# Kernel tuning notes

Hardware: AMD Instinct MI355X
Metric: run time of the kernel (lower is better)

Reference implementation:

```python
import jax, jax.numpy as jnp
import numpy as np

B, C, H, W = 16, 512, 48, 48


def setup_inputs() -> dict:
    key = jax.random.key(0)
    k1, k2 = jax.random.split(key)
    rgb = jax.random.normal(k1, (B, C, H, W), dtype=jnp.float32)
    depth = jax.random.normal(k2, (B, C, H, W), dtype=jnp.float32)
    return {"rgb": rgb, "depth": depth}


def reference(rgb, depth):
    b, c, h, w = rgb.shape
    hw = h * w
    q = rgb.reshape(b, c, hw)              # [B, C, HW]
    k = depth.reshape(b, c, hw)            # [B, C, HW]
    # channel-affinity: energy[b, i, j] = <rgb_chan_i, depth_chan_j>
    energy = jnp.einsum('bcn,bdn->bcd', q, k)   # [B, C, C]
    cl_index = jnp.argmax(energy, axis=2)       # [B, C] best-matching depth channel per rgb channel
    # gather matched depth channels and fuse
    gathered = depth[jnp.arange(b)[:, None], cl_index]  # [B, C, H, W]
    return rgb + gathered
```

## Files before the change

kernel.cpp:

```cpp
#include <hip/hip_runtime.h>
#include <stdint.h>

#define BATCH 16
#define CH    512
#define HW    2304
#define BM    128
#define BN    128

typedef _Float16 half8  __attribute__((ext_vector_type(8)));
typedef float    f32x16 __attribute__((ext_vector_type(16)));

#define MFMA16 __builtin_amdgcn_mfma_f32_32x32x16_f16

#define DELTA 3.5f

#define N_ELEM       ((size_t)BATCH * CH * HW)
#define ENERGY_ELEMS ((size_t)BATCH * CH * CH)
#define WS_FAST16    (ENERGY_ELEMS * 4 + 2 * N_ELEM * 2)

__device__ __forceinline__ uint32_t f32_sortable(float f) {
    uint32_t u = __float_as_uint(f);
    return (u & 0x80000000u) ? ~u : (u | 0x80000000u);
}

__global__ __launch_bounds__(256)
void cvt_f16_kernel(const float* __restrict__ rgb, const float* __restrict__ depth,
                    _Float16* __restrict__ rgb16, _Float16* __restrict__ depth16)
{
    const size_t stride = (size_t)gridDim.x * 256;
    for (size_t i = (size_t)blockIdx.x * 256 + threadIdx.x; i < N_ELEM / 8; i += stride) {
        float4 a0 = ((const float4*)rgb)[2 * i], a1 = ((const float4*)rgb)[2 * i + 1];
        half8 h;
        h[0] = (_Float16)a0.x; h[1] = (_Float16)a0.y;
        h[2] = (_Float16)a0.z; h[3] = (_Float16)a0.w;
        h[4] = (_Float16)a1.x; h[5] = (_Float16)a1.y;
        h[6] = (_Float16)a1.z; h[7] = (_Float16)a1.w;
        ((half8*)rgb16)[i] = h;
        float4 b0 = ((const float4*)depth)[2 * i], b1 = ((const float4*)depth)[2 * i + 1];
        half8 g;
        g[0] = (_Float16)b0.x; g[1] = (_Float16)b0.y;
        g[2] = (_Float16)b0.z; g[3] = (_Float16)b0.w;
        g[4] = (_Float16)b1.x; g[5] = (_Float16)b1.y;
        g[6] = (_Float16)b1.z; g[7] = (_Float16)b1.w;
        ((half8*)depth16)[i] = g;
    }
}


#define BK16    64
#define NKT16   (HW / BK16)
#define A16_OFF 0
#define B16_OFF 16384
#define BUF16_SZ 32768

__device__ __forceinline__ void dma16(const _Float16* g, char* l) {
    __builtin_amdgcn_global_load_lds(
        (const __attribute__((address_space(1))) void*)g,
        (__attribute__((address_space(3))) void*)l, 16, 0, 0);
}

__device__ __forceinline__ half8 rd16(const char* base, int r, int s0) {
    return *(const half8*)(base + r * 128 + ((s0 ^ ((r >> 1) & 7)) << 4));
}

__device__ __forceinline__ void compute16(const char* buf, int rA0, int rB, int hf,
                                          f32x16& acc0, f32x16& acc1) {
    __builtin_amdgcn_s_setprio(1);
    #pragma unroll
    for (int kc = 0; kc < 4; ++kc) {
        const int s0 = 2 * kc + hf;
        half8 a0 = rd16(buf + A16_OFF, rA0,      s0);
        half8 a1 = rd16(buf + A16_OFF, rA0 + 32, s0);
        half8 bb = rd16(buf + B16_OFF, rB,       s0);
        acc0 = MFMA16(a0, bb, acc0, 0, 0, 0);
        acc1 = MFMA16(a1, bb, acc1, 0, 0, 0);
    }
    __builtin_amdgcn_s_setprio(0);
}

__global__ __launch_bounds__(512, 1)
void screen16_kernel(const _Float16* __restrict__ q16,
                     const _Float16* __restrict__ k16,
                     float* __restrict__ energy)
{
    const int bid = blockIdx.x;
    const int nid = (bid & 7) * 32 + (bid >> 3);
    const int d0  = (nid & 3) * BN;
    const int c0  = ((nid >> 2) & 3) * BM;
    const int b   = nid >> 4;

    const int tid  = threadIdx.x;
    const int lane = tid & 63;
    const int w    = tid >> 6;
    const int wm   = w >> 2;
    const int wn   = w & 3;

    __shared__ __align__(16) char sm[2 * BUF16_SZ];

    const _Float16* qb = q16 + (size_t)b * CH * HW;
    const _Float16* kb = k16 + (size_t)b * CH * HW;

    const int lr = lane >> 3, ls = lane & 7;
    const int off0 = lr * HW + ((ls ^ (     (lr >> 1))) << 3);
    const int off1 = lr * HW + ((ls ^ (4 + (lr >> 1))) << 3);
    const _Float16* gA0 = qb + (size_t)(c0 + 16 * w)     * HW + off0;
    const _Float16* gA1 = qb + (size_t)(c0 + 16 * w + 8) * HW + off1;
    const _Float16* gB0 = kb + (size_t)(d0 + 16 * w)     * HW + off0;
    const _Float16* gB1 = kb + (size_t)(d0 + 16 * w + 8) * HW + off1;

    char* ldsA0o = sm + A16_OFF + (16 * w)     * 128;
    char* ldsA1o = sm + A16_OFF + (16 * w + 8) * 128;
    char* ldsB0o = sm + B16_OFF + (16 * w)     * 128;
    char* ldsB1o = sm + B16_OFF + (16 * w + 8) * 128;

    #define DMA_TILE(bufsel, t) do {                    \
        const int ko_ = (t) * BK16;                     \
        const size_t bo_ = (size_t)(bufsel) * BUF16_SZ; \
        dma16(gA0 + ko_, ldsA0o + bo_);                 \
        dma16(gA1 + ko_, ldsA1o + bo_);                 \
        dma16(gB0 + ko_, ldsB0o + bo_);                 \
        dma16(gB1 + ko_, ldsB1o + bo_);                 \
    } while (0)

    DMA_TILE(0, 0);
    DMA_TILE(1, 1);
    asm volatile("s_waitcnt vmcnt(4)" ::: "memory");
    __builtin_amdgcn_sched_barrier(0);
    __builtin_amdgcn_s_barrier();

    f32x16 acc0 = {}, acc1 = {};
    const int rA0 = wm * 64 + (lane & 31);
    const int rB  = wn * 32 + (lane & 31);
    const int hf  = lane >> 5;

    for (int t = 0; t < NKT16; ++t) {
        const char* rdb = sm + (size_t)(t & 1) * BUF16_SZ;
        compute16(rdb, rA0, rB, hf, acc0, acc1);
        if (t == NKT16 - 1) break;
        asm volatile("s_waitcnt lgkmcnt(0)" ::: "memory");
        __builtin_amdgcn_s_barrier();
        __builtin_amdgcn_sched_barrier(0);
        if (t + 2 < NKT16) {
            DMA_TILE(t & 1, t + 2);
            asm volatile("s_waitcnt vmcnt(4)" ::: "memory");
        } else {
            asm volatile("s_waitcnt vmcnt(0)" ::: "memory");
        }
        __builtin_amdgcn_sched_barrier(0);
        __builtin_amdgcn_s_barrier();
    }
    #undef DMA_TILE

    float* eb = energy + ((size_t)(b * CH + c0) * CH) + d0 + wn * 32 + (lane & 31);
    #pragma unroll
    for (int mi = 0; mi < 2; ++mi) {
        #pragma unroll
        for (int qr = 0; qr < 16; ++qr) {
            int rowl = wm * 64 + mi * 32 + (qr & 3) + 8 * (qr >> 2) + 4 * (lane >> 5);
            eb[(size_t)rowl * CH] = (mi == 0) ? acc0[qr] : acc1[qr];
        }
    }
}

__global__ __launch_bounds__(256)
void rescore_gather_kernel(const float* __restrict__ rgb,
                           const float* __restrict__ depth,
                           const float* __restrict__ energy,
                           float* __restrict__ out)
{
    const int row = blockIdx.x;
    const int b   = row >> 9;
    const int tid = threadIdx.x;

    __shared__ float sred[4];
    __shared__ float sM;
    __shared__ int   scnt;
    __shared__ int   slist[CH];
    __shared__ unsigned long long sbest;

    const float* erow = energy + (size_t)row * CH;
    float e0 = erow[tid], e1 = erow[tid + 256];

    float m = fmaxf(e0, e1);
    #pragma unroll
    for (int off = 1; off < 64; off <<= 1) m = fmaxf(m, __shfl_xor(m, off, 64));
    if ((tid & 63) == 0) sred[tid >> 6] = m;
    __syncthreads();
    if (tid == 0) {
        sM = fmaxf(fmaxf(sred[0], sred[1]), fmaxf(sred[2], sred[3]));
        scnt = 0; sbest = 0ull;
    }
    __syncthreads();
    const float thr = sM - DELTA;
    if (e0 >= thr) { int i = atomicAdd(&scnt, 1); slist[i] = tid; }
    if (e1 >= thr) { int i = atomicAdd(&scnt, 1); slist[i] = tid + 256; }
    __syncthreads();
    const int cnt = scnt;

    const float4* q4 = (const float4*)(rgb + (size_t)row * HW);
    for (int i = 0; i < cnt; ++i) {
        const int d = slist[i];
        const float4* k4 = (const float4*)(depth + ((size_t)(b * CH + d)) * HW);
        float s = 0.0f;
        for (int j = tid; j < HW / 4; j += 256) {
            float4 a = q4[j], bb = k4[j];
            s += a.x * bb.x + a.y * bb.y + a.z * bb.z + a.w * bb.w;
        }
        #pragma unroll
        for (int off = 1; off < 64; off <<= 1) s += __shfl_xor(s, off, 64);
        if ((tid & 63) == 0) sred[tid >> 6] = s;
        __syncthreads();
        if (tid == 0) {
            float tot = sred[0] + sred[1] + sred[2] + sred[3];
            unsigned long long p =
                ((unsigned long long)f32_sortable(tot) << 32) |
                (uint32_t)(~(uint32_t)d);
            if (p > sbest) sbest = p;
        }
        __syncthreads();
    }

    const int widx = (int)(~(uint32_t)(sbest & 0xFFFFFFFFull));
    const float4* w4 = (const float4*)(depth + ((size_t)(b * CH + widx)) * HW);
    float4* o4 = (float4*)(out + (size_t)row * HW);
    for (int j = tid; j < HW / 4; j += 256) {
        float4 a = q4[j], dd = w4[j];
        o4[j] = make_float4(a.x + dd.x, a.y + dd.y, a.z + dd.z, a.w + dd.w);
    }
}

#define BKs   64
#define NKTs  (HW / BKs)
#define AHs_OFF 0
#define BHs_OFF 16384
#define BUFs_SZ 32768

#define LGKM_BARRIER() do { \
    asm volatile("s_waitcnt lgkmcnt(0)" ::: "memory"); \
    __builtin_amdgcn_s_barrier(); \
    __builtin_amdgcn_sched_barrier(0); \
} while (0)

__device__ __forceinline__ int swzs(int r, int s) {
    return r * 128 + ((s ^ ((r >> 1) & 7)) << 4);
}

__device__ __forceinline__ half8 cvt8h(const float4& v0, const float4& v1) {
    half8 h;
    h[0] = (_Float16)v0.x; h[1] = (_Float16)v0.y;
    h[2] = (_Float16)v0.z; h[3] = (_Float16)v0.w;
    h[4] = (_Float16)v1.x; h[5] = (_Float16)v1.y;
    h[6] = (_Float16)v1.z; h[7] = (_Float16)v1.w;
    return h;
}

__device__ __forceinline__ void load_tile_s(const float* aG, const float* bG, int k0,
                                            float4 (&av)[4], float4 (&bv)[4]) {
    av[0] = *(const float4*)(aG + k0 + 0);
    av[1] = *(const float4*)(aG + k0 + 4);
    av[2] = *(const float4*)(aG + k0 + 8);
    av[3] = *(const float4*)(aG + k0 + 12);
    bv[0] = *(const float4*)(bG + k0 + 0);
    bv[1] = *(const float4*)(bG + k0 + 4);
    bv[2] = *(const float4*)(bG + k0 + 8);
    bv[3] = *(const float4*)(bG + k0 + 12);
}

__device__ __forceinline__ void stage_tile_s(char* dst,
                                             const float4 (&av)[4], const float4 (&bv)[4],
                                             int row, int q) {
    *(half8*)(dst + AHs_OFF + swzs(row, 2 * q))     = cvt8h(av[0], av[1]);
    *(half8*)(dst + AHs_OFF + swzs(row, 2 * q + 1)) = cvt8h(av[2], av[3]);
    *(half8*)(dst + BHs_OFF + swzs(row, 2 * q))     = cvt8h(bv[0], bv[1]);
    *(half8*)(dst + BHs_OFF + swzs(row, 2 * q + 1)) = cvt8h(bv[2], bv[3]);
}

__device__ __forceinline__ void compute_tile_s(const char* buf, int rA0, int rB, int half,
                                               f32x16& acc0, f32x16& acc1) {
    __builtin_amdgcn_s_setprio(1);
    #pragma unroll
    for (int kc = 0; kc < 4; ++kc) {
        const int s0 = 2 * kc + half;
        half8 ah0 = *(const half8*)(buf + AHs_OFF + swzs(rA0,      s0));
        half8 ah1 = *(const half8*)(buf + AHs_OFF + swzs(rA0 + 32, s0));
        half8 bh  = *(const half8*)(buf + BHs_OFF + swzs(rB, s0));
        acc0 = MFMA16(ah0, bh, acc0, 0, 0, 0);
        acc1 = MFMA16(ah1, bh, acc1, 0, 0, 0);
    }
    __builtin_amdgcn_s_setprio(0);
}

__global__ __launch_bounds__(512, 1)
void screen_kernel(const float* __restrict__ q,
                   const float* __restrict__ kmat,
                   float* __restrict__ energy)
{
    const int bid = blockIdx.x;
    const int nid = (bid & 7) * 32 + (bid >> 3);
    const int d0  = (nid & 3) * BN;
    const int c0  = ((nid >> 2) & 3) * BM;
    const int b   = nid >> 4;

    const int tid  = threadIdx.x;
    const int lane = tid & 63;
    const int w    = tid >> 6;
    const int wm   = w >> 2;
    const int wn   = w & 3;

    __shared__ __align__(16) char sm[2 * BUFs_SZ];
    char* buf0 = sm;
    char* buf1 = sm + BUFs_SZ;

    const float* qb = q    + (size_t)b * CH * HW;
    const float* kb = kmat + (size_t)b * CH * HW;

    const int row = tid >> 2, sq = tid & 3;
    const float* aG = qb + (size_t)(c0 + row) * HW + sq * 16;
    const float* bG = kb + (size_t)(d0 + row) * HW + sq * 16;

    float4 av0[4], bv0[4], av1[4], bv1[4];

    load_tile_s(aG, bG, 0, av0, bv0);
    stage_tile_s(buf0, av0, bv0, row, sq);
    load_tile_s(aG, bG, BKs, av1, bv1);
    LGKM_BARRIER();

    f32x16 acc0 = {}, acc1 = {};
    const int rA0  = wm * 64 + (lane & 31);
    const int rB   = wn * 32 + (lane & 31);
    const int half = lane >> 5;

    for (int kt = 0; kt < NKTs; kt += 2) {
        if (kt + 2 < NKTs) load_tile_s(aG, bG, (kt + 2) * BKs, av0, bv0);
        stage_tile_s(buf1, av1, bv1, row, sq);
        compute_tile_s(buf0, rA0, rB, half, acc0, acc1);
        LGKM_BARRIER();
        if (kt + 3 < NKTs) load_tile_s(aG, bG, (kt + 3) * BKs, av1, bv1);
        if (kt + 2 < NKTs) stage_tile_s(buf0, av0, bv0, row, sq);
        compute_tile_s(buf1, rA0, rB, half, acc0, acc1);
        LGKM_BARRIER();
    }

    float* eb = energy + ((size_t)(b * CH + c0) * CH) + d0 + wn * 32 + (lane & 31);
    #pragma unroll
    for (int mi = 0; mi < 2; ++mi) {
        #pragma unroll
        for (int qr = 0; qr < 16; ++qr) {
            int rowl = wm * 64 + mi * 32 + (qr & 3) + 8 * (qr >> 2) + 4 * (lane >> 5);
            eb[(size_t)rowl * CH] = (mi == 0) ? acc0[qr] : acc1[qr];
        }
    }
}

extern "C" void kernel_launch(void* const* d_in, const int* in_sizes, int n_in,
                              void* d_out, int out_size, void* d_ws, size_t ws_size,
                              hipStream_t stream)
{
    const float* rgb   = (const float*)d_in[0];
    const float* depth = (const float*)d_in[1];
    float* out = (float*)d_out;
    float* energy = (float*)d_ws;

    if (ws_size >= WS_FAST16) {
        _Float16* rgb16   = (_Float16*)((char*)d_ws + ENERGY_ELEMS * 4);
        _Float16* depth16 = rgb16 + N_ELEM;
        cvt_f16_kernel<<<2048, 256, 0, stream>>>(rgb, depth, rgb16, depth16);
        screen16_kernel<<<256, 512, 0, stream>>>(rgb16, depth16, energy);
        rescore_gather_kernel<<<BATCH * CH, 256, 0, stream>>>(rgb, depth, energy, out);
    } else {
        screen_kernel<<<256, 512, 0, stream>>>(rgb, depth, energy);
        rescore_gather_kernel<<<BATCH * CH, 256, 0, stream>>>(rgb, depth, energy, out);
    }
}
```

Baseline: 123.1 us.

## Replace f16 pre-convert pass with split-K 256x256 screen kernel fusing conversion

Drops the separate fp32-to-fp16 conversion kernel and the DMA-based 128x128 screen kernel. The new screen kernel loads fp32 directly, converts it in registers and stages it to LDS. It uses 256x256 output tiles with 8 MFMA accumulators per wave and splits the K dimension 4 ways, so there are still 256 blocks. The partial energies go to four workspace slices, and the rescore kernel sums them before the argmax screening. The goal is to remove the conversion pass's extra memory traffic and to improve operand reuse. In exchange it writes and reads 4x the energy traffic and uses 128KB of LDS with launch_bounds(512,2), which may limit occupancy or increase register pressure.

```diff
diff --git a/kernel.cpp b/kernel.cpp
--- a/kernel.cpp
+++ b/kernel.cpp
@@ -4,8 +4,6 @@
 #define BATCH 16
 #define CH    512
 #define HW    2304
-#define BM    128
-#define BN    128
 
 typedef _Float16 half8  __attribute__((ext_vector_type(8)));
 typedef float    f32x16 __attribute__((ext_vector_type(16)));
@@ -14,150 +12,142 @@
 
 #define DELTA 3.5f
 
-#define N_ELEM       ((size_t)BATCH * CH * HW)
 #define ENERGY_ELEMS ((size_t)BATCH * CH * CH)
-#define WS_FAST16    (ENERGY_ELEMS * 4 + 2 * N_ELEM * 2)
+#define KSP     4
+#define WS_NEED (KSP * ENERGY_ELEMS * 4)
+
+#define LGKM_BARRIER() do { \
+    asm volatile("s_waitcnt lgkmcnt(0)" ::: "memory"); \
+    __builtin_amdgcn_s_barrier(); \
+    __builtin_amdgcn_sched_barrier(0); \
+} while (0)
 
 __device__ __forceinline__ uint32_t f32_sortable(float f) {
     uint32_t u = __float_as_uint(f);
     return (u & 0x80000000u) ? ~u : (u | 0x80000000u);
 }
 
-__global__ __launch_bounds__(256)
-void cvt_f16_kernel(const float* __restrict__ rgb, const float* __restrict__ depth,
-                    _Float16* __restrict__ rgb16, _Float16* __restrict__ depth16)
-{
-    const size_t stride = (size_t)gridDim.x * 256;
-    for (size_t i = (size_t)blockIdx.x * 256 + threadIdx.x; i < N_ELEM / 8; i += stride) {
-        float4 a0 = ((const float4*)rgb)[2 * i], a1 = ((const float4*)rgb)[2 * i + 1];
-        half8 h;
-        h[0] = (_Float16)a0.x; h[1] = (_Float16)a0.y;
-        h[2] = (_Float16)a0.z; h[3] = (_Float16)a0.w;
-        h[4] = (_Float16)a1.x; h[5] = (_Float16)a1.y;
-        h[6] = (_Float16)a1.z; h[7] = (_Float16)a1.w;
-        ((half8*)rgb16)[i] = h;
-        float4 b0 = ((const float4*)depth)[2 * i], b1 = ((const float4*)depth)[2 * i + 1];
-        half8 g;
-        g[0] = (_Float16)b0.x; g[1] = (_Float16)b0.y;
-        g[2] = (_Float16)b0.z; g[3] = (_Float16)b0.w;
-        g[4] = (_Float16)b1.x; g[5] = (_Float16)b1.y;
-        g[6] = (_Float16)b1.z; g[7] = (_Float16)b1.w;
-        ((half8*)depth16)[i] = g;
-    }
-}
-
-
-#define BK16    64
-#define NKT16   (HW / BK16)
-#define A16_OFF 0
-#define B16_OFF 16384
-#define BUF16_SZ 32768
-
-__device__ __forceinline__ void dma16(const _Float16* g, char* l) {
-    __builtin_amdgcn_global_load_lds(
-        (const __attribute__((address_space(1))) void*)g,
-        (__attribute__((address_space(3))) void*)l, 16, 0, 0);
-}
-
-__device__ __forceinline__ half8 rd16(const char* base, int r, int s0) {
-    return *(const half8*)(base + r * 128 + ((s0 ^ ((r >> 1) & 7)) << 4));
-}
-
-__device__ __forceinline__ void compute16(const char* buf, int rA0, int rB, int hf,
-                                          f32x16& acc0, f32x16& acc1) {
+__device__ __forceinline__ int swzs(int r, int s) {
+    return r * 128 + ((s ^ ((r >> 1) & 7)) << 4);
+}
+
+__device__ __forceinline__ half8 cvt8h(const float4& v0, const float4& v1) {
+    half8 h;
+    h[0] = (_Float16)v0.x; h[1] = (_Float16)v0.y;
+    h[2] = (_Float16)v0.z; h[3] = (_Float16)v0.w;
+    h[4] = (_Float16)v1.x; h[5] = (_Float16)v1.y;
+    h[6] = (_Float16)v1.z; h[7] = (_Float16)v1.w;
+    return h;
+}
+
+#define BK3   64
+#define KRANGE (HW / KSP)
+#define NST   (KRANGE / BK3)
+#define A3_OFF 0
+#define B3_OFF 32768
+#define BUF3_SZ 65536
+
+__device__ __forceinline__ void load_tile3(const float* aT, const float* bT,
+                                           float4 (&av)[8], float4 (&bv)[8]) {
+    #pragma unroll
+    for (int i = 0; i < 8; ++i) av[i] = *(const float4*)(aT + 4 * i);
+    #pragma unroll
+    for (int i = 0; i < 8; ++i) bv[i] = *(const float4*)(bT + 4 * i);
+}
+
+__device__ __forceinline__ void stage_tile3(char* dst,
+                                            const float4 (&av)[8], const float4 (&bv)[8],
+                                            int arow, int ah) {
+    #pragma unroll
+    for (int j = 0; j < 4; ++j)
+        *(half8*)(dst + A3_OFF + swzs(arow, 4 * ah + j)) = cvt8h(av[2 * j], av[2 * j + 1]);
+    #pragma unroll
+    for (int j = 0; j < 4; ++j)
+        *(half8*)(dst + B3_OFF + swzs(arow, 4 * ah + j)) = cvt8h(bv[2 * j], bv[2 * j + 1]);
+}
+
+__device__ __forceinline__ void compute_tile3(const char* buf, int rA0, int rB0, int hf,
+                                              f32x16 (&acc)[2][4]) {
     __builtin_amdgcn_s_setprio(1);
     #pragma unroll
     for (int kc = 0; kc < 4; ++kc) {
         const int s0 = 2 * kc + hf;
-        half8 a0 = rd16(buf + A16_OFF, rA0,      s0);
-        half8 a1 = rd16(buf + A16_OFF, rA0 + 32, s0);
-        half8 bb = rd16(buf + B16_OFF, rB,       s0);
-        acc0 = MFMA16(a0, bb, acc0, 0, 0, 0);
-        acc1 = MFMA16(a1, bb, acc1, 0, 0, 0);
+        half8 a0 = *(const half8*)(buf + A3_OFF + swzs(rA0,      s0));
+        half8 a1 = *(const half8*)(buf + A3_OFF + swzs(rA0 + 32, s0));
+        half8 b0 = *(const half8*)(buf + B3_OFF + swzs(rB0,      s0));
+        half8 b1 = *(const half8*)(buf + B3_OFF + swzs(rB0 + 32, s0));
+        half8 b2 = *(const half8*)(buf + B3_OFF + swzs(rB0 + 64, s0));
+        half8 b3 = *(const half8*)(buf + B3_OFF + swzs(rB0 + 96, s0));
+        acc[0][0] = MFMA16(a0, b0, acc[0][0], 0, 0, 0);
+        acc[0][1] = MFMA16(a0, b1, acc[0][1], 0, 0, 0);
+        acc[0][2] = MFMA16(a0, b2, acc[0][2], 0, 0, 0);
+        acc[0][3] = MFMA16(a0, b3, acc[0][3], 0, 0, 0);
+        acc[1][0] = MFMA16(a1, b0, acc[1][0], 0, 0, 0);
+        acc[1][1] = MFMA16(a1, b1, acc[1][1], 0, 0, 0);
+        acc[1][2] = MFMA16(a1, b2, acc[1][2], 0, 0, 0);
+        acc[1][3] = MFMA16(a1, b3, acc[1][3], 0, 0, 0);
     }
     __builtin_amdgcn_s_setprio(0);
 }
 
-__global__ __launch_bounds__(512, 1)
-void screen16_kernel(const _Float16* __restrict__ q16,
-                     const _Float16* __restrict__ k16,
-                     float* __restrict__ energy)
+__global__ __launch_bounds__(512, 2)
+void screen3_kernel(const float* __restrict__ q,
+                    const float* __restrict__ kmat,
+                    float* __restrict__ epart)
 {
     const int bid = blockIdx.x;
     const int nid = (bid & 7) * 32 + (bid >> 3);
-    const int d0  = (nid & 3) * BN;
-    const int c0  = ((nid >> 2) & 3) * BM;
+    const int ks  = nid & 3;
+    const int d0  = ((nid >> 2) & 1) * 256;
+    const int c0  = ((nid >> 3) & 1) * 256;
     const int b   = nid >> 4;
+    const int kbase = ks * KRANGE;
 
     const int tid  = threadIdx.x;
     const int lane = tid & 63;
     const int w    = tid >> 6;
-    const int wm   = w >> 2;
-    const int wn   = w & 3;
-
-    __shared__ __align__(16) char sm[2 * BUF16_SZ];
-
-    const _Float16* qb = q16 + (size_t)b * CH * HW;
-    const _Float16* kb = k16 + (size_t)b * CH * HW;
-
-    const int lr = lane >> 3, ls = lane & 7;
-    const int off0 = lr * HW + ((ls ^ (     (lr >> 1))) << 3);
-    const int off1 = lr * HW + ((ls ^ (4 + (lr >> 1))) << 3);
-    const _Float16* gA0 = qb + (size_t)(c0 + 16 * w)     * HW + off0;
-    const _Float16* gA1 = qb + (size_t)(c0 + 16 * w + 8) * HW + off1;
-    const _Float16* gB0 = kb + (size_t)(d0 + 16 * w)     * HW + off0;
-    const _Float16* gB1 = kb + (size_t)(d0 + 16 * w + 8) * HW + off1;
-
-    char* ldsA0o = sm + A16_OFF + (16 * w)     * 128;
-    char* ldsA1o = sm + A16_OFF + (16 * w + 8) * 128;
-    char* ldsB0o = sm + B16_OFF + (16 * w)     * 128;
-    char* ldsB1o = sm + B16_OFF + (16 * w + 8) * 128;
-
-    #define DMA_TILE(bufsel, t) do {                    \
-        const int ko_ = (t) * BK16;                     \
-        const size_t bo_ = (size_t)(bufsel) * BUF16_SZ; \
-        dma16(gA0 + ko_, ldsA0o + bo_);                 \
-        dma16(gA1 + ko_, ldsA1o + bo_);                 \
-        dma16(gB0 + ko_, ldsB0o + bo_);                 \
-        dma16(gB1 + ko_, ldsB1o + bo_);                 \
-    } while (0)
-
-    DMA_TILE(0, 0);
-    DMA_TILE(1, 1);
-    asm volatile("s_waitcnt vmcnt(4)" ::: "memory");
-    __builtin_amdgcn_sched_barrier(0);
-    __builtin_amdgcn_s_barrier();
-
-    f32x16 acc0 = {}, acc1 = {};
+    const int wm   = w >> 1;
+    const int wn   = w & 1;
+
+    __shared__ __align__(16) char sm[2 * BUF3_SZ];
+
+    const int arow = tid >> 1, ah = tid & 1;
+    const float* aG = q    + ((size_t)b * CH + c0 + arow) * HW + kbase + ah * 32;
+    const float* bG = kmat + ((size_t)b * CH + d0 + arow) * HW + kbase + ah * 32;
+
+    float4 av[8], bv[8];
+
+    load_tile3(aG, bG, av, bv);
+    stage_tile3(sm, av, bv, arow, ah);
+    load_tile3(aG + BK3, bG + BK3, av, bv);
+    LGKM_BARRIER();
+
+    f32x16 acc[2][4] = {};
     const int rA0 = wm * 64 + (lane & 31);
-    const int rB  = wn * 32 + (lane & 31);
+    const int rB0 = wn * 128 + (lane & 31);
     const int hf  = lane >> 5;
 
-    for (int t = 0; t < NKT16; ++t) {
-        const char* rdb = sm + (size_t)(t & 1) * BUF16_SZ;
-        compute16(rdb, rA0, rB, hf, acc0, acc1);
-        if (t == NKT16 - 1) break;
-        asm volatile("s_waitcnt lgkmcnt(0)" ::: "memory");
-        __builtin_amdgcn_s_barrier();
-        __builtin_amdgcn_sched_barrier(0);
-        if (t + 2 < NKT16) {
-            DMA_TILE(t & 1, t + 2);
-            asm volatile("s_waitcnt vmcnt(4)" ::: "memory");
-        } else {
-            asm volatile("s_waitcnt vmcnt(0)" ::: "memory");
-        }
-        __builtin_amdgcn_sched_barrier(0);
-        __builtin_amdgcn_s_barrier();
-    }
-    #undef DMA_TILE
-
-    float* eb = energy + ((size_t)(b * CH + c0) * CH) + d0 + wn * 32 + (lane & 31);
+    for (int t = 0; t < NST; ++t) {
+        compute_tile3(sm + (size_t)(t & 1) * BUF3_SZ, rA0, rB0, hf, acc);
+        if (t + 1 < NST) {
+            stage_tile3(sm + (size_t)((t + 1) & 1) * BUF3_SZ, av, bv, arow, ah);
+            LGKM_BARRIER();
+            if (t + 2 < NST)
+                load_tile3(aG + (t + 2) * BK3, bG + (t + 2) * BK3, av, bv);
+        }
+    }
+
+    float* eb = epart + (size_t)ks * ENERGY_ELEMS
+              + ((size_t)(b * CH + c0) * CH) + d0 + wn * 128 + (lane & 31);
     #pragma unroll
     for (int mi = 0; mi < 2; ++mi) {
         #pragma unroll
-        for (int qr = 0; qr < 16; ++qr) {
-            int rowl = wm * 64 + mi * 32 + (qr & 3) + 8 * (qr >> 2) + 4 * (lane >> 5);
-            eb[(size_t)rowl * CH] = (mi == 0) ? acc0[qr] : acc1[qr];
+        for (int ni = 0; ni < 4; ++ni) {
+            #pragma unroll
+            for (int qr = 0; qr < 16; ++qr) {
+                int rowl = wm * 64 + mi * 32 + (qr & 3) + 8 * (qr >> 2) + 4 * (lane >> 5);
+                eb[(size_t)rowl * CH + ni * 32] = acc[mi][ni][qr];
+            }
         }
     }
 }
@@ -166,6 +156,7 @@
 void rescore_gather_kernel(const float* __restrict__ rgb,
                            const float* __restrict__ depth,
                            const float* __restrict__ energy,
+                           int np,
                            float* __restrict__ out)
 {
     const int row = blockIdx.x;
@@ -179,7 +170,11 @@
     __shared__ unsigned long long sbest;
 
     const float* erow = energy + (size_t)row * CH;
-    float e0 = erow[tid], e1 = erow[tid + 256];
+    float e0 = 0.0f, e1 = 0.0f;
+    for (int p = 0; p < np; ++p) {
+        e0 += erow[(size_t)p * ENERGY_ELEMS + tid];
+        e1 += erow[(size_t)p * ENERGY_ELEMS + tid + 256];
+    }
 
     float m = fmaxf(e0, e1);
     #pragma unroll
@@ -235,25 +230,6 @@
 #define BHs_OFF 16384
 #define BUFs_SZ 32768
 
-#define LGKM_BARRIER() do { \
-    asm volatile("s_waitcnt lgkmcnt(0)" ::: "memory"); \
-    __builtin_amdgcn_s_barrier(); \
-    __builtin_amdgcn_sched_barrier(0); \
-} while (0)
-
-__device__ __forceinline__ int swzs(int r, int s) {
-    return r * 128 + ((s ^ ((r >> 1) & 7)) << 4);
-}
-
-__device__ __forceinline__ half8 cvt8h(const float4& v0, const float4& v1) {
-    half8 h;
-    h[0] = (_Float16)v0.x; h[1] = (_Float16)v0.y;
-    h[2] = (_Float16)v0.z; h[3] = (_Float16)v0.w;
-    h[4] = (_Float16)v1.x; h[5] = (_Float16)v1.y;
-    h[6] = (_Float16)v1.z; h[7] = (_Float16)v1.w;
-    return h;
-}
-
 __device__ __forceinline__ void load_tile_s(const float* aG, const float* bG, int k0,
                                             float4 (&av)[4], float4 (&bv)[4]) {
     av[0] = *(const float4*)(aG + k0 + 0);
@@ -297,8 +273,8 @@
 {
     const int bid = blockIdx.x;
     const int nid = (bid & 7) * 32 + (bid >> 3);
-    const int d0  = (nid & 3) * BN;
-    const int c0  = ((nid >> 2) & 3) * BM;
+    const int d0  = (nid & 3) * 128;
+    const int c0  = ((nid >> 2) & 3) * 128;
     const int b   = nid >> 4;
 
     const int tid  = threadIdx.x;
@@ -361,14 +337,11 @@
     float* out = (float*)d_out;
     float* energy = (float*)d_ws;
 
-    if (ws_size >= WS_FAST16) {
-        _Float16* rgb16   = (_Float16*)((char*)d_ws + ENERGY_ELEMS * 4);
-        _Float16* depth16 = rgb16 + N_ELEM;
-        cvt_f16_kernel<<<2048, 256, 0, stream>>>(rgb, depth, rgb16, depth16);
-        screen16_kernel<<<256, 512, 0, stream>>>(rgb16, depth16, energy);
-        rescore_gather_kernel<<<BATCH * CH, 256, 0, stream>>>(rgb, depth, energy, out);
+    if (ws_size >= WS_NEED) {
+        screen3_kernel<<<256, 512, 0, stream>>>(rgb, depth, energy);
+        rescore_gather_kernel<<<BATCH * CH, 256, 0, stream>>>(rgb, depth, energy, KSP, out);
     } else {
         screen_kernel<<<256, 512, 0, stream>>>(rgb, depth, energy);
-        rescore_gather_kernel<<<BATCH * CH, 256, 0, stream>>>(rgb, depth, energy, out);
-    }
-}
+        rescore_gather_kernel<<<BATCH * CH, 256, 0, stream>>>(rgb, depth, energy, 1, out);
+    }
+}
```

Result: faster. 116.0 us (-5.8%).
